# Optimization experiments

Hardware: AMD Instinct MI355X
Metric: run time of the kernel (lower is better)

## Reference

```python
import jax, jax.numpy as jnp
import numpy as np

N = 8192
QS = 128
KS = 128
F = 256
EPS = 1e-5     # BatchNorm1d default eps
SLOPE = 0.01   # LeakyReLU default negative_slope


def _leaky(x):
    return jnp.where(x >= 0, x, SLOPE * x)


def _mlp_bn(x, w1, b1, w2, b2, gamma, beta):
    # Sequential(Linear, LeakyReLU, Linear, LeakyReLU) then BatchNorm1d (training mode)
    h = _leaky(x @ w1 + b1)
    h = _leaky(h @ w2 + b2)
    mean = h.mean(axis=0)
    var = h.var(axis=0)  # biased variance, as torch BN uses for normalization
    return gamma * (h - mean) * jax.lax.rsqrt(var + EPS) + beta


def setup_inputs() -> dict:
    key = jax.random.key(0)
    ks = jax.random.split(key, 24)

    def lin_w(k_, fi, fo):
        s = 1.0 / np.sqrt(fi)
        return jax.random.uniform(k_, (fi, fo), minval=-s, maxval=s, dtype=jnp.float32)

    def lin_b(k_, fi, fo):
        s = 1.0 / np.sqrt(fi)
        return jax.random.uniform(k_, (fo,), minval=-s, maxval=s, dtype=jnp.float32)

    A = (jax.random.uniform(ks[0], (N, N)) < 0.004).astype(jnp.float32)
    q = jax.random.normal(ks[1], (N, QS), dtype=jnp.float32)
    k = jax.random.normal(ks[2], (N, KS), dtype=jnp.float32)

    inp = {"A": A, "q": q, "k": k}
    i = 3
    for pre, fi in (("q", QS), ("k", KS), ("v", KS)):
        inp[pre + "_w1"] = lin_w(ks[i], fi, F); i += 1
        inp[pre + "_b1"] = lin_b(ks[i], fi, F); i += 1
        inp[pre + "_w2"] = lin_w(ks[i], F, F); i += 1
        inp[pre + "_b2"] = lin_b(ks[i], F, F); i += 1
        inp[pre + "_gamma"] = jnp.ones((F,), jnp.float32)
        inp[pre + "_beta"] = jnp.zeros((F,), jnp.float32)
    return inp


def reference(A, q, k,
              q_w1, q_b1, q_w2, q_b2, q_gamma, q_beta,
              k_w1, k_b1, k_w2, k_b2, k_gamma, k_beta,
              v_w1, v_b1, v_w2, v_b2, v_gamma, v_beta):
    qe1 = _mlp_bn(q, q_w1, q_b1, q_w2, q_b2, q_gamma, q_beta)   # [N, F]
    ke1 = _mlp_bn(k, k_w1, k_b1, k_w2, k_b2, k_gamma, k_beta)   # [N, F]
    prod = (qe1 @ ke1.T) / jnp.sqrt(jnp.float32(F))             # [N, N]
    # NOTE: faithful to source — mask zeroes scores (not -inf) before softmax
    masked = A * prod
    attn = jax.nn.softmax(masked, axis=1)
    ve1 = _mlp_bn(k, v_w1, v_b1, v_w2, v_b2, v_gamma, v_beta)   # [N, F]
    return attn @ ve1                                            # [N, F]
```

## Files before the change

kernel.cpp:

```cpp
#include <hip/hip_runtime.h>

#define NROWS 8192
#define FDIM 256
#define CAP 128

typedef _Float16 half8_t __attribute__((ext_vector_type(8)));
typedef _Float16 half4_t __attribute__((ext_vector_type(4)));
typedef float floatx4 __attribute__((ext_vector_type(4)));

struct MlpPtrs {
  const float* w1[3]; const float* b1[3];
  const float* w2[3]; const float* b2[3];
  const float* gamma[3]; const float* beta[3];
};

__device__ __forceinline__ void scan_row(
    int r, int lane, int wave, const float* __restrict__ A,
    int* __restrict__ colidx, int* __restrict__ rowcnt,
    int (&sj)[4][CAP], int (&cnt)[4]) {
  if (lane == 0) cnt[wave] = 0;
  const floatx4* row = (const floatx4*)(A + (size_t)r * NROWS);
  for (int b = 0; b < 4; ++b) {
    floatx4 av[8];
    #pragma unroll
    for (int it = 0; it < 8; ++it)
      av[it] = __builtin_nontemporal_load(&row[(b * 8 + it) * 64 + lane]);
    #pragma unroll
    for (int it = 0; it < 8; ++it) {
      int base = ((b * 8 + it) * 64 + lane) * 4;
      int cols[4]; int c = 0;
      if (av[it][0] != 0.f) cols[c++] = base + 0;
      if (av[it][1] != 0.f) cols[c++] = base + 1;
      if (av[it][2] != 0.f) cols[c++] = base + 2;
      if (av[it][3] != 0.f) cols[c++] = base + 3;
      if (c) {
        int pos = atomicAdd(&cnt[wave], c);
        for (int l = 0; l < c; ++l) if (pos + l < CAP) sj[wave][pos + l] = cols[l];
      }
    }
  }
  int nnz = cnt[wave] < CAP ? cnt[wave] : CAP;
  if (lane < nnz) colidx[(size_t)r * CAP + lane] = sj[wave][lane];
  if (lane + 64 < nnz) colidx[(size_t)r * CAP + lane + 64] = sj[wave][lane + 64];
  if (lane == 0) rowcnt[r] = nnz;
}

__global__ __launch_bounds__(256) void prep_kernel(
    MlpPtrs p, _Float16* __restrict__ w1p, _Float16* __restrict__ w2p) {
  int task = blockIdx.y;
  int tid = blockIdx.x * 256 + threadIdx.x;
  int m = task % 3;
  bool isw2 = task >= 3;
  int K = isw2 ? 256 : 128;
  if (tid >= K * 256) return;
  const float* src = isw2 ? p.w2[m] : p.w1[m];
  _Float16* dst = isw2 ? (w2p + m * 65536) : (w1p + m * 32768);
  int j = tid & 7, lane = (tid >> 3) & 63, rest = tid >> 9;
  int ktiles = K >> 5;
  int k_tile = rest % ktiles, n_tile = rest / ktiles;
  int kk = k_tile * 32 + (lane >> 4) * 8 + j;
  int nn = n_tile * 16 + (lane & 15);
  dst[tid] = (_Float16)src[kk * 256 + nn];
}

__global__ __launch_bounds__(256) void gemm1_kernel(
    const float* __restrict__ q, const float* __restrict__ k,
    const _Float16* __restrict__ w1p, MlpPtrs p, _Float16* __restrict__ h1,
    const float* __restrict__ A, int* __restrict__ colidx, int* __restrict__ rowcnt) {
  __shared__ int sj[4][CAP];
  __shared__ int cnt[4];
  int lane = threadIdx.x & 63, wave = threadIdx.x >> 6;
  int bid = blockIdx.x;
  if (bid < 1024) {
    scan_row(bid * 4 + wave, lane, wave, A, colidx, rowcnt, sj, cnt);
    return;
  }
  int t = bid - 1024;
  int z = t / 512, rem = t % 512, by = rem / 128, bx = rem % 128;
  const float* X = (z == 0) ? q : k;
  const _Float16* wp = w1p + z * 32768;
  _Float16* out = h1 + (size_t)z * (NROWS * FDIM);
  const float* bias = p.b1[z];
  int lm = lane & 15, lq = lane >> 4;
  int m0 = bx * 64 + wave * 16;
  int n0 = by * 64;
  floatx4 acc[4];
  #pragma unroll
  for (int u = 0; u < 4; ++u) acc[u] = (floatx4){0.f, 0.f, 0.f, 0.f};
  const float* ap = X + (size_t)(m0 + lm) * 128 + lq * 8;
  const half8_t* wp8 = (const half8_t*)wp;
  #pragma unroll
  for (int kt = 0; kt < 4; ++kt) {
    floatx4 a0 = *(const floatx4*)(ap + kt * 32);
    floatx4 a1 = *(const floatx4*)(ap + kt * 32 + 4);
    half8_t a = (half8_t){(_Float16)a0[0], (_Float16)a0[1], (_Float16)a0[2], (_Float16)a0[3],
                          (_Float16)a1[0], (_Float16)a1[1], (_Float16)a1[2], (_Float16)a1[3]};
    #pragma unroll
    for (int u = 0; u < 4; ++u) {
      half8_t b = wp8[(((n0 >> 4) + u) * 4 + kt) * 64 + lane];
      acc[u] = __builtin_amdgcn_mfma_f32_16x16x32_f16(a, b, acc[u], 0, 0, 0);
    }
  }
  #pragma unroll
  for (int u = 0; u < 4; ++u) {
    int col = n0 + u * 16 + lm;
    float bb = bias[col];
    #pragma unroll
    for (int r = 0; r < 4; ++r) {
      float v = acc[u][r] + bb;
      v = (v >= 0.f) ? v : 0.01f * v;
      out[(size_t)(m0 + lq * 4 + r) * FDIM + col] = (_Float16)v;
    }
  }
}

__global__ __launch_bounds__(256) void gemm2_kernel(
    const _Float16* __restrict__ h1, const _Float16* __restrict__ w2p,
    MlpPtrs p, _Float16* __restrict__ e1,
    float* __restrict__ colsum, float* __restrict__ colsumsq,
    const float* __restrict__ A, int* __restrict__ colidx, int* __restrict__ rowcnt) {
  __shared__ int sj[4][CAP];
  __shared__ int cnt[4];
  int lane = threadIdx.x & 63, wave = threadIdx.x >> 6;
  int bid = blockIdx.x;
  if (bid < 1024) {
    scan_row(4096 + bid * 4 + wave, lane, wave, A, colidx, rowcnt, sj, cnt);
    return;
  }
  int t = bid - 1024;
  int z = t / 512, rem = t % 512, by = rem / 128, bx = rem % 128;
  const _Float16* X = h1 + (size_t)z * (NROWS * FDIM);
  const _Float16* wp = w2p + z * 65536;
  _Float16* out = e1 + (size_t)z * (NROWS * FDIM);
  const float* bias = p.b2[z];
  int lm = lane & 15, lq = lane >> 4;
  int m0 = bx * 64 + wave * 16;
  int n0 = by * 64;
  floatx4 acc[4];
  #pragma unroll
  for (int u = 0; u < 4; ++u) acc[u] = (floatx4){0.f, 0.f, 0.f, 0.f};
  const half8_t* ap = (const half8_t*)(X + (size_t)(m0 + lm) * 256 + lq * 8);
  const half8_t* wp8 = (const half8_t*)wp;
  #pragma unroll
  for (int kt = 0; kt < 8; ++kt) {
    half8_t a = ap[kt * 4];
    #pragma unroll
    for (int u = 0; u < 4; ++u) {
      half8_t b = wp8[(((n0 >> 4) + u) * 8 + kt) * 64 + lane];
      acc[u] = __builtin_amdgcn_mfma_f32_16x16x32_f16(a, b, acc[u], 0, 0, 0);
    }
  }
  #pragma unroll
  for (int u = 0; u < 4; ++u) {
    int col = n0 + u * 16 + lm;
    float bb = bias[col];
    float s = 0.f, s2 = 0.f;
    #pragma unroll
    for (int r = 0; r < 4; ++r) {
      float v = acc[u][r] + bb;
      v = (v >= 0.f) ? v : 0.01f * v;
      out[(size_t)(m0 + lq * 4 + r) * FDIM + col] = (_Float16)v;
      s += v; s2 += v * v;
    }
    s  += __shfl_xor(s, 16, 64);  s  += __shfl_xor(s, 32, 64);
    s2 += __shfl_xor(s2, 16, 64); s2 += __shfl_xor(s2, 32, 64);
    if (lq == 0) {
      atomicAdd(&colsum[z * FDIM + col], s);
      atomicAdd(&colsumsq[z * FDIM + col], s2);
    }
  }
}

__global__ __launch_bounds__(256) void stats_kernel(
    const float* __restrict__ colsum, const float* __restrict__ colsumsq,
    MlpPtrs p, float* __restrict__ scaleA, float* __restrict__ shiftA) {
  int c = threadIdx.x;
  #pragma unroll
  for (int m = 0; m < 3; ++m) {
    float mean = colsum[m * FDIM + c] * (1.f / NROWS);
    float var = colsumsq[m * FDIM + c] * (1.f / NROWS) - mean * mean;
    float sc = p.gamma[m][c] * rsqrtf(var + 1e-5f);
    scaleA[m * FDIM + c] = sc;
    shiftA[m * FDIM + c] = p.beta[m][c] - mean * sc;
  }
}

__global__ __launch_bounds__(256) void attn_kernel(
    const int* __restrict__ colidx, const int* __restrict__ rowcnt,
    const _Float16* __restrict__ e1,
    const float* __restrict__ scaleA, const float* __restrict__ shiftA,
    const float* __restrict__ colsum, float* __restrict__ out) {
  const _Float16* qe = e1;
  const _Float16* ke = e1 + (size_t)1 * NROWS * FDIM;
  const _Float16* ve = e1 + (size_t)2 * NROWS * FDIM;
  int lane = threadIdx.x & 63, wave = threadIdx.x >> 6;
  int i = blockIdx.x * 4 + wave;
  __shared__ int sj[4][CAP];
  __shared__ float sw[4][CAP];

  int nnz = rowcnt[i];
  if (lane < nnz) sj[wave][lane] = colidx[(size_t)i * CAP + lane];
  if (lane + 64 < nnz) sj[wave][lane + 64] = colidx[(size_t)i * CAP + lane + 64];

  int cl = lane & 15, g = lane >> 4;
  const half8_t* qp = (const half8_t*)(qe + (size_t)i * FDIM + cl * 16);
  half8_t qa = qp[0], qb8 = qp[1];
  const floatx4* sq4 = (const floatx4*)(scaleA + cl * 16);
  const floatx4* hq4 = (const floatx4*)(shiftA + cl * 16);
  const floatx4* sk4 = (const floatx4*)(scaleA + FDIM + cl * 16);
  const floatx4* hk4 = (const floatx4*)(shiftA + FDIM + cl * 16);
  float qk[16]; float qb = 0.f;
  #pragma unroll
  for (int v4 = 0; v4 < 4; ++v4) {
    floatx4 sq = sq4[v4], hq = hq4[v4], sk = sk4[v4], hk = hk4[v4];
    #pragma unroll
    for (int r = 0; r < 4; ++r) {
      int c = v4 * 4 + r;
      float qr = (c < 8) ? (float)qa[c] : (float)qb8[c - 8];
      float qn = qr * sq[r] + hq[r];
      qk[c] = qn * sk[r] * 0.0625f;
      qb += qn * hk[r] * 0.0625f;
    }
  }

  for (int e = g; e < nnz; e += 4) {
    int j = sj[wave][e];
    const half8_t* kp = (const half8_t*)(ke + (size_t)j * FDIM + cl * 16);
    half8_t ka = kp[0], kb = kp[1];
    float s = qb;
    #pragma unroll
    for (int r = 0; r < 8; ++r)
      s += qk[r] * (float)ka[r] + qk[r + 8] * (float)kb[r];
    #pragma unroll
    for (int off = 8; off >= 1; off >>= 1) s += __shfl_xor(s, off, 64);
    if (cl == 0) sw[wave][e] = s;
  }

  float v0 = lane < nnz ? sw[wave][lane] : 0.f;
  float v1 = lane + 64 < nnz ? sw[wave][lane + 64] : 0.f;
  float m = fmaxf(fmaxf(v0, v1), 0.f);
  #pragma unroll
  for (int off = 32; off >= 1; off >>= 1) m = fmaxf(m, __shfl_xor(m, off, 64));
  float em = __expf(-m);
  float w0 = lane < nnz ? __expf(v0 - m) : 0.f;
  float w1 = lane + 64 < nnz ? __expf(v1 - m) : 0.f;
  float ls = w0 + w1;
  #pragma unroll
  for (int off = 32; off >= 1; off >>= 1) ls += __shfl_xor(ls, off, 64);
  if (lane < nnz) sw[wave][lane] = w0 - em;
  if (lane + 64 < nnz) sw[wave][lane + 64] = w1 - em;
  float wsum = ls - (float)nnz * em;
  float inv = 1.f / (ls + (float)(NROWS - nnz) * em);

  floatx4 acc = (floatx4){0.f, 0.f, 0.f, 0.f};
  for (int e = 0; e < nnz; ++e) {
    int j = sj[wave][e];
    float w = sw[wave][e];
    half4_t vv = *(const half4_t*)(ve + (size_t)j * FDIM + lane * 4);
    acc[0] += w * (float)vv[0]; acc[1] += w * (float)vv[1];
    acc[2] += w * (float)vv[2]; acc[3] += w * (float)vv[3];
  }

  floatx4 sv = *(const floatx4*)(scaleA + 2 * FDIM + lane * 4);
  floatx4 sh = *(const floatx4*)(shiftA + 2 * FDIM + lane * 4);
  floatx4 cs = *(const floatx4*)(colsum + 2 * FDIM + lane * 4);
  float bg = wsum + em * (float)NROWS;
  floatx4 o;
  #pragma unroll
  for (int r = 0; r < 4; ++r)
    o[r] = inv * (sv[r] * (acc[r] + em * cs[r]) + sh[r] * bg);
  __builtin_nontemporal_store(o, (floatx4*)(out + (size_t)i * FDIM + lane * 4));
}

extern "C" void kernel_launch(void* const* d_in, const int* in_sizes, int n_in,
                              void* d_out, int out_size, void* d_ws, size_t ws_size,
                              hipStream_t stream) {
  const float* A = (const float*)d_in[0];
  const float* q = (const float*)d_in[1];
  const float* k = (const float*)d_in[2];
  MlpPtrs p;
  for (int m = 0; m < 3; ++m) {
    const int b = 3 + m * 6;
    p.w1[m]    = (const float*)d_in[b + 0];
    p.b1[m]    = (const float*)d_in[b + 1];
    p.w2[m]    = (const float*)d_in[b + 2];
    p.b2[m]    = (const float*)d_in[b + 3];
    p.gamma[m] = (const float*)d_in[b + 4];
    p.beta[m]  = (const float*)d_in[b + 5];
  }
  char* ws = (char*)d_ws;
  const size_t MB = 1024 * 1024;
  _Float16* h1  = (_Float16*)(ws + 0);
  _Float16* e1  = (_Float16*)(ws + 12 * MB);
  _Float16* w1p = (_Float16*)(ws + 24 * MB);
  _Float16* w2p = (_Float16*)(ws + 24 * MB + 192 * 1024);
  float* colsum   = (float*)(ws + 25 * MB);
  float* colsumsq = colsum + 3 * FDIM;
  float* scaleA   = colsumsq + 3 * FDIM;
  float* shiftA   = scaleA + 3 * FDIM;
  int* colidx = (int*)(ws + 26 * MB);
  int* rowcnt = (int*)(ws + 30 * MB);

  (void)hipMemsetAsync(colsum, 0, 2 * 3 * FDIM * sizeof(float), stream);
  prep_kernel<<<dim3(256, 6, 1), 256, 0, stream>>>(p, w1p, w2p);
  gemm1_kernel<<<1024 + 1536, 256, 0, stream>>>(q, k, w1p, p, h1, A, colidx, rowcnt);
  gemm2_kernel<<<1024 + 1536, 256, 0, stream>>>(h1, w2p, p, e1, colsum, colsumsq, A, colidx, rowcnt);
  stats_kernel<<<1, 256, 0, stream>>>(colsum, colsumsq, p, scaleA, shiftA);
  attn_kernel<<<NROWS / 4, 256, 0, stream>>>(colidx, rowcnt, e1, scaleA, shiftA, colsum, (float*)d_out);
}
```

Measured before the change: 454.4 us.

## Fuse both MLP GEMMs into one kernel with shared-memory hidden tile

Merges the two MLP layer kernels into one. Each block computes a 64-row by 256-column hidden tile, keeps it in LDS in fp16 and runs the second GEMM from there, so the h1 intermediate never goes to global memory. The adjacency scan moves entirely into this kernel's leading 2048 blocks, each loading a whole row into 32 registers at once. The separate stats kernel is removed: every attention block recomputes the BN scale and shift into shared memory. The cost is fewer, heavier GEMM blocks (384), higher register pressure from the 4x4 accumulators and the 32-vector scan loads, and redundant stats work in every attention block.

New measurement: 426.7 us. -6.1%, faster.

```diff
diff --git a/kernel.cpp b/kernel.cpp
--- a/kernel.cpp
+++ b/kernel.cpp
@@ -17,26 +17,24 @@
 __device__ __forceinline__ void scan_row(
     int r, int lane, int wave, const float* __restrict__ A,
     int* __restrict__ colidx, int* __restrict__ rowcnt,
-    int (&sj)[4][CAP], int (&cnt)[4]) {
+    int (*sj)[CAP], int* cnt) {
   if (lane == 0) cnt[wave] = 0;
   const floatx4* row = (const floatx4*)(A + (size_t)r * NROWS);
-  for (int b = 0; b < 4; ++b) {
-    floatx4 av[8];
-    #pragma unroll
-    for (int it = 0; it < 8; ++it)
-      av[it] = __builtin_nontemporal_load(&row[(b * 8 + it) * 64 + lane]);
-    #pragma unroll
-    for (int it = 0; it < 8; ++it) {
-      int base = ((b * 8 + it) * 64 + lane) * 4;
-      int cols[4]; int c = 0;
-      if (av[it][0] != 0.f) cols[c++] = base + 0;
-      if (av[it][1] != 0.f) cols[c++] = base + 1;
-      if (av[it][2] != 0.f) cols[c++] = base + 2;
-      if (av[it][3] != 0.f) cols[c++] = base + 3;
-      if (c) {
-        int pos = atomicAdd(&cnt[wave], c);
-        for (int l = 0; l < c; ++l) if (pos + l < CAP) sj[wave][pos + l] = cols[l];
-      }
+  floatx4 av[32];
+  #pragma unroll
+  for (int it = 0; it < 32; ++it)
+    av[it] = __builtin_nontemporal_load(&row[it * 64 + lane]);
+  #pragma unroll
+  for (int it = 0; it < 32; ++it) {
+    int base = (it * 64 + lane) * 4;
+    int cols[4]; int c = 0;
+    if (av[it][0] != 0.f) cols[c++] = base + 0;
+    if (av[it][1] != 0.f) cols[c++] = base + 1;
+    if (av[it][2] != 0.f) cols[c++] = base + 2;
+    if (av[it][3] != 0.f) cols[c++] = base + 3;
+    if (c) {
+      int pos = atomicAdd(&cnt[wave], c);
+      for (int l = 0; l < c; ++l) if (pos + l < CAP) sj[wave][pos + l] = cols[l];
     }
   }
   int nnz = cnt[wave] < CAP ? cnt[wave] : CAP;
@@ -63,104 +61,108 @@
   dst[tid] = (_Float16)src[kk * 256 + nn];
 }
 
-__global__ __launch_bounds__(256) void gemm1_kernel(
+__global__ __launch_bounds__(256) void mlp_kernel(
     const float* __restrict__ q, const float* __restrict__ k,
-    const _Float16* __restrict__ w1p, MlpPtrs p, _Float16* __restrict__ h1,
+    const _Float16* __restrict__ w1p, const _Float16* __restrict__ w2p, MlpPtrs p,
+    _Float16* __restrict__ e1, float* __restrict__ colsum, float* __restrict__ colsumsq,
     const float* __restrict__ A, int* __restrict__ colidx, int* __restrict__ rowcnt) {
-  __shared__ int sj[4][CAP];
-  __shared__ int cnt[4];
+  __shared__ __align__(16) char smraw[64 * 264 * 2];
   int lane = threadIdx.x & 63, wave = threadIdx.x >> 6;
   int bid = blockIdx.x;
-  if (bid < 1024) {
+  if (bid < 2048) {
+    int (*sj)[CAP] = (int (*)[CAP])smraw;
+    int* cnt = (int*)(smraw + sizeof(int) * 4 * CAP);
     scan_row(bid * 4 + wave, lane, wave, A, colidx, rowcnt, sj, cnt);
     return;
   }
-  int t = bid - 1024;
-  int z = t / 512, rem = t % 512, by = rem / 128, bx = rem % 128;
+  _Float16 (*hT)[264] = (_Float16 (*)[264])smraw;
+  int t = bid - 2048;
+  int z = t % 3, bx = t / 3;
+  int m0 = bx * 64;
   const float* X = (z == 0) ? q : k;
-  const _Float16* wp = w1p + z * 32768;
-  _Float16* out = h1 + (size_t)z * (NROWS * FDIM);
-  const float* bias = p.b1[z];
+  const half8_t* w1p8 = (const half8_t*)(w1p + z * 32768);
+  const half8_t* w2p8 = (const half8_t*)(w2p + z * 65536);
   int lm = lane & 15, lq = lane >> 4;
-  int m0 = bx * 64 + wave * 16;
-  int n0 = by * 64;
-  floatx4 acc[4];
-  #pragma unroll
-  for (int u = 0; u < 4; ++u) acc[u] = (floatx4){0.f, 0.f, 0.f, 0.f};
-  const float* ap = X + (size_t)(m0 + lm) * 128 + lq * 8;
-  const half8_t* wp8 = (const half8_t*)wp;
+
+  floatx4 acc[4][4];
+  #pragma unroll
+  for (int a = 0; a < 4; ++a)
+    #pragma unroll
+    for (int b = 0; b < 4; ++b) acc[a][b] = (floatx4){0.f, 0.f, 0.f, 0.f};
+
+  const float* xp = X + (size_t)(m0 + lm) * 128 + lq * 8;
   #pragma unroll
   for (int kt = 0; kt < 4; ++kt) {
-    floatx4 a0 = *(const floatx4*)(ap + kt * 32);
-    floatx4 a1 = *(const floatx4*)(ap + kt * 32 + 4);
-    half8_t a = (half8_t){(_Float16)a0[0], (_Float16)a0[1], (_Float16)a0[2], (_Float16)a0[3],
-                          (_Float16)a1[0], (_Float16)a1[1], (_Float16)a1[2], (_Float16)a1[3]};
+    half8_t xf[4];
+    #pragma unroll
+    for (int rr = 0; rr < 4; ++rr) {
+      floatx4 a0 = *(const floatx4*)(xp + rr * 16 * 128 + kt * 32);
+      floatx4 a1 = *(const floatx4*)(xp + rr * 16 * 128 + kt * 32 + 4);
+      xf[rr] = (half8_t){(_Float16)a0[0], (_Float16)a0[1], (_Float16)a0[2], (_Float16)a0[3],
+                         (_Float16)a1[0], (_Float16)a1[1], (_Float16)a1[2], (_Float16)a1[3]};
+    }
     #pragma unroll
     for (int u = 0; u < 4; ++u) {
-      half8_t b = wp8[(((n0 >> 4) + u) * 4 + kt) * 64 + lane];
-      acc[u] = __builtin_amdgcn_mfma_f32_16x16x32_f16(a, b, acc[u], 0, 0, 0);
-    }
-  }
+      half8_t wf = w1p8[((wave * 4 + u) * 4 + kt) * 64 + lane];
+      #pragma unroll
+      for (int rr = 0; rr < 4; ++rr)
+        acc[rr][u] = __builtin_amdgcn_mfma_f32_16x16x32_f16(wf, xf[rr], acc[rr][u], 0, 0, 0);
+    }
+  }
+  {
+    const float* b1 = p.b1[z];
+    #pragma unroll
+    for (int u = 0; u < 4; ++u) {
+      floatx4 bb = *(const floatx4*)(b1 + (wave * 4 + u) * 16 + lq * 4);
+      #pragma unroll
+      for (int rr = 0; rr < 4; ++rr) {
+        half4_t hv;
+        #pragma unroll
+        for (int r = 0; r < 4; ++r) {
+          float v = acc[rr][u][r] + bb[r];
+          v = (v >= 0.f) ? v : 0.01f * v;
+          hv[r] = (_Float16)v;
+        }
+        *(half4_t*)(&hT[rr * 16 + lm][(wave * 4 + u) * 16 + lq * 4]) = hv;
+      }
+    }
+  }
+  __syncthreads();
+
+  #pragma unroll
+  for (int a = 0; a < 4; ++a)
+    #pragma unroll
+    for (int b = 0; b < 4; ++b) acc[a][b] = (floatx4){0.f, 0.f, 0.f, 0.f};
+  #pragma unroll
+  for (int kt = 0; kt < 8; ++kt) {
+    half8_t af[4];
+    #pragma unroll
+    for (int rr = 0; rr < 4; ++rr)
+      af[rr] = *(const half8_t*)(&hT[rr * 16 + lm][kt * 32 + lq * 8]);
+    #pragma unroll
+    for (int u = 0; u < 4; ++u) {
+      half8_t bf = w2p8[((wave * 4 + u) * 8 + kt) * 64 + lane];
+      #pragma unroll
+      for (int rr = 0; rr < 4; ++rr)
+        acc[rr][u] = __builtin_amdgcn_mfma_f32_16x16x32_f16(af[rr], bf, acc[rr][u], 0, 0, 0);
+    }
+  }
+  const float* b2 = p.b2[z];
+  _Float16* out = e1 + (size_t)z * (NROWS * FDIM);
   #pragma unroll
   for (int u = 0; u < 4; ++u) {
-    int col = n0 + u * 16 + lm;
-    float bb = bias[col];
-    #pragma unroll
-    for (int r = 0; r < 4; ++r) {
-      float v = acc[u][r] + bb;
-      v = (v >= 0.f) ? v : 0.01f * v;
-      out[(size_t)(m0 + lq * 4 + r) * FDIM + col] = (_Float16)v;
-    }
-  }
-}
-
-__global__ __launch_bounds__(256) void gemm2_kernel(
-    const _Float16* __restrict__ h1, const _Float16* __restrict__ w2p,
-    MlpPtrs p, _Float16* __restrict__ e1,
-    float* __restrict__ colsum, float* __restrict__ colsumsq,
-    const float* __restrict__ A, int* __restrict__ colidx, int* __restrict__ rowcnt) {
-  __shared__ int sj[4][CAP];
-  __shared__ int cnt[4];
-  int lane = threadIdx.x & 63, wave = threadIdx.x >> 6;
-  int bid = blockIdx.x;
-  if (bid < 1024) {
-    scan_row(4096 + bid * 4 + wave, lane, wave, A, colidx, rowcnt, sj, cnt);
-    return;
-  }
-  int t = bid - 1024;
-  int z = t / 512, rem = t % 512, by = rem / 128, bx = rem % 128;
-  const _Float16* X = h1 + (size_t)z * (NROWS * FDIM);
-  const _Float16* wp = w2p + z * 65536;
-  _Float16* out = e1 + (size_t)z * (NROWS * FDIM);
-  const float* bias = p.b2[z];
-  int lm = lane & 15, lq = lane >> 4;
-  int m0 = bx * 64 + wave * 16;
-  int n0 = by * 64;
-  floatx4 acc[4];
-  #pragma unroll
-  for (int u = 0; u < 4; ++u) acc[u] = (floatx4){0.f, 0.f, 0.f, 0.f};
-  const half8_t* ap = (const half8_t*)(X + (size_t)(m0 + lm) * 256 + lq * 8);
-  const half8_t* wp8 = (const half8_t*)wp;
-  #pragma unroll
-  for (int kt = 0; kt < 8; ++kt) {
-    half8_t a = ap[kt * 4];
-    #pragma unroll
-    for (int u = 0; u < 4; ++u) {
-      half8_t b = wp8[(((n0 >> 4) + u) * 8 + kt) * 64 + lane];
-      acc[u] = __builtin_amdgcn_mfma_f32_16x16x32_f16(a, b, acc[u], 0, 0, 0);
-    }
-  }
-  #pragma unroll
-  for (int u = 0; u < 4; ++u) {
-    int col = n0 + u * 16 + lm;
-    float bb = bias[col];
+    int col = wave * 64 + u * 16 + lm;
+    float bb = b2[col];
     float s = 0.f, s2 = 0.f;
     #pragma unroll
-    for (int r = 0; r < 4; ++r) {
-      float v = acc[u][r] + bb;
-      v = (v >= 0.f) ? v : 0.01f * v;
-      out[(size_t)(m0 + lq * 4 + r) * FDIM + col] = (_Float16)v;
-      s += v; s2 += v * v;
+    for (int rr = 0; rr < 4; ++rr) {
+      #pragma unroll
+      for (int r = 0; r < 4; ++r) {
+        float v = acc[rr][u][r] + bb;
+        v = (v >= 0.f) ? v : 0.01f * v;
+        out[(size_t)(m0 + rr * 16 + lq * 4 + r) * FDIM + col] = (_Float16)v;
+        s += v; s2 += v * v;
+      }
     }
     s  += __shfl_xor(s, 16, 64);  s  += __shfl_xor(s, 32, 64);
     s2 += __shfl_xor(s2, 16, 64); s2 += __shfl_xor(s2, 32, 64);
@@ -171,25 +173,11 @@
   }
 }
 
-__global__ __launch_bounds__(256) void stats_kernel(
-    const float* __restrict__ colsum, const float* __restrict__ colsumsq,
-    MlpPtrs p, float* __restrict__ scaleA, float* __restrict__ shiftA) {
-  int c = threadIdx.x;
-  #pragma unroll
-  for (int m = 0; m < 3; ++m) {
-    float mean = colsum[m * FDIM + c] * (1.f / NROWS);
-    float var = colsumsq[m * FDIM + c] * (1.f / NROWS) - mean * mean;
-    float sc = p.gamma[m][c] * rsqrtf(var + 1e-5f);
-    scaleA[m * FDIM + c] = sc;
-    shiftA[m * FDIM + c] = p.beta[m][c] - mean * sc;
-  }
-}
-
 __global__ __launch_bounds__(256) void attn_kernel(
     const int* __restrict__ colidx, const int* __restrict__ rowcnt,
     const _Float16* __restrict__ e1,
-    const float* __restrict__ scaleA, const float* __restrict__ shiftA,
-    const float* __restrict__ colsum, float* __restrict__ out) {
+    const float* __restrict__ colsum, const float* __restrict__ colsumsq,
+    MlpPtrs p, float* __restrict__ out) {
   const _Float16* qe = e1;
   const _Float16* ke = e1 + (size_t)1 * NROWS * FDIM;
   const _Float16* ve = e1 + (size_t)2 * NROWS * FDIM;
@@ -197,18 +185,32 @@
   int i = blockIdx.x * 4 + wave;
   __shared__ int sj[4][CAP];
   __shared__ float sw[4][CAP];
-
+  __shared__ __align__(16) float sscale[3 * FDIM];
+  __shared__ __align__(16) float sshift[3 * FDIM];
+
+  {
+    int c = threadIdx.x;
+    #pragma unroll
+    for (int m = 0; m < 3; ++m) {
+      float mean = colsum[m * FDIM + c] * (1.f / NROWS);
+      float var = colsumsq[m * FDIM + c] * (1.f / NROWS) - mean * mean;
+      float sc = p.gamma[m][c] * rsqrtf(var + 1e-5f);
+      sscale[m * FDIM + c] = sc;
+      sshift[m * FDIM + c] = p.beta[m][c] - mean * sc;
+    }
+  }
   int nnz = rowcnt[i];
   if (lane < nnz) sj[wave][lane] = colidx[(size_t)i * CAP + lane];
   if (lane + 64 < nnz) sj[wave][lane + 64] = colidx[(size_t)i * CAP + lane + 64];
+  __syncthreads();
 
   int cl = lane & 15, g = lane >> 4;
   const half8_t* qp = (const half8_t*)(qe + (size_t)i * FDIM + cl * 16);
   half8_t qa = qp[0], qb8 = qp[1];
-  const floatx4* sq4 = (const floatx4*)(scaleA + cl * 16);
-  const floatx4* hq4 = (const floatx4*)(shiftA + cl * 16);
-  const floatx4* sk4 = (const floatx4*)(scaleA + FDIM + cl * 16);
-  const floatx4* hk4 = (const floatx4*)(shiftA + FDIM + cl * 16);
+  const floatx4* sq4 = (const floatx4*)(sscale + cl * 16);
+  const floatx4* hq4 = (const floatx4*)(sshift + cl * 16);
+  const floatx4* sk4 = (const floatx4*)(sscale + FDIM + cl * 16);
+  const floatx4* hk4 = (const floatx4*)(sshift + FDIM + cl * 16);
   float qk[16]; float qb = 0.f;
   #pragma unroll
   for (int v4 = 0; v4 < 4; ++v4) {
@@ -261,8 +263,8 @@
     acc[2] += w * (float)vv[2]; acc[3] += w * (float)vv[3];
   }
 
-  floatx4 sv = *(const floatx4*)(scaleA + 2 * FDIM + lane * 4);
-  floatx4 sh = *(const floatx4*)(shiftA + 2 * FDIM + lane * 4);
+  floatx4 sv = *(const floatx4*)(sscale + 2 * FDIM + lane * 4);
+  floatx4 sh = *(const floatx4*)(sshift + 2 * FDIM + lane * 4);
   floatx4 cs = *(const floatx4*)(colsum + 2 * FDIM + lane * 4);
   float bg = wsum + em * (float)NROWS;
   floatx4 o;
@@ -290,21 +292,18 @@
   }
   char* ws = (char*)d_ws;
   const size_t MB = 1024 * 1024;
-  _Float16* h1  = (_Float16*)(ws + 0);
-  _Float16* e1  = (_Float16*)(ws + 12 * MB);
-  _Float16* w1p = (_Float16*)(ws + 24 * MB);
-  _Float16* w2p = (_Float16*)(ws + 24 * MB + 192 * 1024);
-  float* colsum   = (float*)(ws + 25 * MB);
+  _Float16* e1  = (_Float16*)(ws + 0);
+  _Float16* w1p = (_Float16*)(ws + 12 * MB);
+  _Float16* w2p = (_Float16*)(ws + 12 * MB + 512 * 1024);
+  float* colsum   = (float*)(ws + 13 * MB);
   float* colsumsq = colsum + 3 * FDIM;
-  float* scaleA   = colsumsq + 3 * FDIM;
-  float* shiftA   = scaleA + 3 * FDIM;
-  int* colidx = (int*)(ws + 26 * MB);
-  int* rowcnt = (int*)(ws + 30 * MB);
+  int* colidx = (int*)(ws + 14 * MB);
+  int* rowcnt = (int*)(ws + 18 * MB);
 
   (void)hipMemsetAsync(colsum, 0, 2 * 3 * FDIM * sizeof(float), stream);
   prep_kernel<<<dim3(256, 6, 1), 256, 0, stream>>>(p, w1p, w2p);
-  gemm1_kernel<<<1024 + 1536, 256, 0, stream>>>(q, k, w1p, p, h1, A, colidx, rowcnt);
-  gemm2_kernel<<<1024 + 1536, 256, 0, stream>>>(h1, w2p, p, e1, colsum, colsumsq, A, colidx, rowcnt);
-  stats_kernel<<<1, 256, 0, stream>>>(colsum, colsumsq, p, scaleA, shiftA);
-  attn_kernel<<<NROWS / 4, 256, 0, stream>>>(colidx, rowcnt, e1, scaleA, shiftA, colsum, (float*)d_out);
-}
+  mlp_kernel<<<2048 + 384, 256, 0, stream>>>(q, k, w1p, w2p, p, e1, colsum, colsumsq,
+                                             A, colidx, rowcnt);
+  attn_kernel<<<NROWS / 4, 256, 0, stream>>>(colidx, rowcnt, e1, colsum, colsumsq, p,
+                                             (float*)d_out);
+}
```
